# Kernel optimization log

Measured on AMD Instinct MI355X. Metric: run time of the kernel, lower is better.

The kernel has to match this reference:

```python
import jax, jax.numpy as jnp
import numpy as np

# hyperparameters (from init_kwargs / repo defaults)
AMP_COEF = 1.0
ARG_COEF = 1.0
SSIM_COEF = 1.0
BETA = 1.0
STFT_COEF = 1e-4
EPS = 1e-8
STFT_F = 12
STFT_S = 4


def _gauss_kernel(size=11, sigma=1.5):
    x = jnp.arange(size, dtype=jnp.float32) - (size - 1) / 2.0
    g = jnp.exp(-0.5 * (x / sigma) ** 2)
    k = jnp.outer(g, g)
    return k / jnp.sum(k)


def _depthwise_filter(img, k):
    # img: [B,H,W,C]; 11x11 gaussian, VALID padding, depthwise (per-channel)
    c = img.shape[-1]
    kern = jnp.tile(k[:, :, None, None], (1, 1, 1, c))  # HWIO, I=1, O=C
    return jax.lax.conv_general_dilated(
        img, kern, (1, 1), 'VALID',
        dimension_numbers=('NHWC', 'HWIO', 'NHWC'),
        feature_group_count=c)


def ssim(x, y, max_val=1.0):
    # faithful to tf.image.ssim defaults: filter 11, sigma 1.5, k1=0.01, k2=0.03
    c1 = (0.01 * max_val) ** 2
    c2 = (0.03 * max_val) ** 2
    k = _gauss_kernel()
    mu_x = _depthwise_filter(x, k)
    mu_y = _depthwise_filter(y, k)
    var_x = _depthwise_filter(x * x, k) - mu_x * mu_x
    var_y = _depthwise_filter(y * y, k) - mu_y * mu_y
    cov = _depthwise_filter(x * y, k) - mu_x * mu_y
    lum = (2.0 * mu_x * mu_y + c1) / (mu_x * mu_x + mu_y * mu_y + c1)
    cs = (2.0 * cov + c2) / (var_x + var_y + c2)
    return jnp.mean(lum * cs, axis=(1, 2, 3))  # [B]


def stft(image, f=STFT_F, s=STFT_S):
    # image: [B,N,N,C] -> batched patchwise 2D FFT, cropped to [:f//2,:f//2]
    n = image.shape[1]
    p = (n - f) // s + 1          # num_conv per axis
    half = f // 2
    rows = (jnp.arange(p) * s)[:, None] + jnp.arange(f)   # [P, f]
    patches = image[:, rows]                              # [B,P,f,N,C]
    patches = patches[:, :, :, rows]                      # [B,P,f,P,f,C]
    patches = jnp.transpose(patches, (0, 1, 3, 2, 4, 5))  # [B,Pi,Pj,f,f,C]
    b, c = image.shape[0], image.shape[-1]
    patches = patches.reshape(b, p * p, f, f, c)          # k = i*P + j ordering
    fft = jnp.fft.fft2(patches.astype(jnp.complex64), axes=(2, 3))
    return fft[:, :, :half, :half, :]                     # [B,P*P,half,half,C]


def _freq_filter(f=STFT_F):
    lin = jnp.linspace(0.0, 1.0, f // 2)[:, None]
    return (lin * lin.T)[:, :, None]                      # [half,half,1]


def setup_inputs() -> dict:
    key = jax.random.key(0)
    k1, k2, k3, k4 = jax.random.split(key, 4)
    B, N, C, L = 32, 160, 3, 128
    return {
        'mean': jax.random.normal(k1, (B, L), dtype=jnp.float32),
        'logvar': jax.random.normal(k2, (B, L), dtype=jnp.float32),
        'x_in': jax.random.uniform(k3, (B, N, N, C), dtype=jnp.float32),
        'x_out': jax.random.uniform(k4, (B, N, N, C), dtype=jnp.float32),
    }


def reference(mean, logvar, x_in, x_out):
    # KLD per sample
    var = jnp.exp(logvar)
    kld = -0.5 * jnp.sum(1.0 + logvar - var - mean * mean, axis=1)  # [B]
    # SSIM recon term
    recons = SSIM_COEF * ssim(x_in, x_out, 1.0)                     # [B]
    # patchwise STFT amp/phase loss ('ours')
    stft_out = stft(x_out, STFT_F, STFT_S)
    stft_in = stft(x_in, STFT_F, STFT_S)
    ff = _freq_filter(STFT_F)                                       # [half,half,1]
    arg_diff = jnp.abs(jnp.angle(stft_out + EPS) - jnp.angle(stft_in + EPS))
    amp_diff = jnp.abs(jnp.abs(stft_out) - jnp.abs(stft_in))
    arg_loss = jnp.sum(arg_diff * ff, axis=(1, 2, 3, 4))            # [B]
    amp_loss = jnp.sum(amp_diff * ff, axis=(1, 2, 3, 4))            # [B]
    stft_loss = ARG_COEF * arg_loss + AMP_COEF * amp_loss
    loss = jnp.mean(BETA * kld + recons + STFT_COEF * stft_loss)
    return loss
```

## Files before the change

kernel.cpp:

```cpp
#include <hip/hip_runtime.h>
#include <hip/hip_fp16.h>
#include <math.h>

#define BATCH 32
#define NPIX 160
#define LDIM 128
#define OUT_SZ 150

#define THREADS 512
#define N_BLOCKS 1825
#define SCRATCH_OFF 2880
#define VSTRIDE 1296
#define SMEM_FLOATS 9360

__device__ constexpr float TWC[12] = { 1.f, 0.86602540f, 0.5f, 0.f, -0.5f, -0.86602540f,
                                      -1.f,-0.86602540f,-0.5f, 0.f,  0.5f,  0.86602540f};
__device__ constexpr float TWS[12] = { 0.f,-0.5f,-0.86602540f,-1.f,-0.86602540f,-0.5f,
                                       0.f, 0.5f, 0.86602540f, 1.f, 0.86602540f, 0.5f};

__device__ constexpr float GW[11] = {0.00102838f, 0.00759876f, 0.03600076f, 0.10936070f,
                                     0.21300554f, 0.26601172f, 0.21300554f, 0.10936070f,
                                     0.03600076f, 0.00759876f, 0.00102838f};

__device__ __forceinline__ float fast_atan2f(float y, float x) {
    float ax = fabsf(x), ay = fabsf(y);
    float mx = fmaxf(ax, ay), mn = fminf(ax, ay);
    float z = mn * __builtin_amdgcn_rcpf(mx);
    float z2 = z * z;
    float p = fmaf(z2, -0.01172120f, 0.05265332f);
    p = fmaf(z2, p, -0.11643287f);
    p = fmaf(z2, p, 0.19354346f);
    p = fmaf(z2, p, -0.33262347f);
    p = fmaf(z2, p, 0.99997726f);
    p = p * z;
    if (ay > ax) p = 1.57079632679489662f - p;
    if (x < 0.f) p = 3.14159265358979323f - p;
    return (y < 0.f) ? -p : p;
}

__device__ __forceinline__ float4 extract_c(float4 f0, float4 f1, float4 f2, int c) {
    if (c == 0) return make_float4(f0.x, f0.w, f1.z, f2.y);
    if (c == 1) return make_float4(f0.y, f1.x, f1.w, f2.z);
    return make_float4(f0.z, f1.y, f2.x, f2.w);
}

__global__ __launch_bounds__(THREADS) void work_kernel(const float* __restrict__ xin,
                                                       const float* __restrict__ xout,
                                                       const float* __restrict__ mean,
                                                       const float* __restrict__ logvar,
                                                       float* __restrict__ out) {
    __shared__ __align__(16) float SMEM[SMEM_FLOATS];
    __shared__ float sm8[8];
    const int tid = threadIdx.x;
    const int gid = blockIdx.x;
    float acc = 0.f;

    if (gid == 1824) {
        float a = 0.f;
        for (int i = tid; i < BATCH * LDIM; i += THREADS) {
            float m = mean[i], lv = logvar[i];
            a += -0.5f * (1.f + lv - expf(lv) - m * m) * (1.f / 32.f);
        }
        #pragma unroll
        for (int o = 32; o > 0; o >>= 1) a += __shfl_down(a, o, 64);
        if ((tid & 63) == 0) sm8[tid >> 6] = a;
        __syncthreads();
        if (tid == 0) {
            float s = sm8[0];
            #pragma unroll
            for (int i = 1; i < 8; ++i) s += sm8[i];
            atomicAdd(out, s);
        }
        return;
    }

    int b    = gid / 57;
    int rem  = gid % 57;
    int c    = rem / 19;
    int tile = rem % 19;
    int r0 = tile * 8;
    __half2* HXY = (__half2*)SMEM;
    __half2* RD  = (__half2*)(SMEM + SCRATCH_OFF);

    for (int t = tid; t < 720; t += THREADS) {
        int rr = t / 40;
        int cq = t % 40;
        int row = r0 + rr;
        float4 xa = make_float4(0.f, 0.f, 0.f, 0.f);
        float4 xb = make_float4(0.f, 0.f, 0.f, 0.f);
        if (row < NPIX) {
            size_t off = ((size_t)(b * 160 + row) * 160 + cq * 4) * 3;
            const float4* qa = (const float4*)(xin + off);
            const float4* qb = (const float4*)(xout + off);
            float4 a0 = qa[0], a1 = qa[1], a2 = qa[2];
            float4 b0 = qb[0], b1 = qb[1], b2 = qb[2];
            xa = extract_c(a0, a1, a2, c);
            xb = extract_c(b0, b1, b2, c);
        }
        __half2 h[4] __attribute__((aligned(16)));
        h[0] = __floats2half2_rn(xa.x, xb.x);
        h[1] = __floats2half2_rn(xa.y, xb.y);
        h[2] = __floats2half2_rn(xa.z, xb.z);
        h[3] = __floats2half2_rn(xa.w, xb.w);
        *(float4*)&HXY[rr * 160 + cq * 4] = *(float4*)h;
    }
    __syncthreads();

    for (int t = tid; t < 608; t += THREADS) {
        int pc = t % 38;
        int r  = t / 38;
        float4 raw[3];
        raw[0] = *(const float4*)&HXY[r * 160 + pc * 4];
        raw[1] = *(const float4*)&HXY[r * 160 + pc * 4 + 4];
        raw[2] = *(const float4*)&HXY[r * 160 + pc * 4 + 8];
        const __half2* hp = (const __half2*)raw;
        float xa[12], xb[12];
        #pragma unroll
        for (int j = 0; j < 12; ++j) {
            float2 xy = __half22float2(hp[j]);
            xa[j] = xy.x; xb[j] = xy.y;
        }
        float evA[5] = {xa[1]+xa[11], xa[2]+xa[10], xa[3]+xa[9], xa[4]+xa[8], xa[5]+xa[7]};
        float ovA[5] = {xa[1]-xa[11], xa[2]-xa[10], xa[3]-xa[9], xa[4]-xa[8], xa[5]-xa[7]};
        float evB[5] = {xb[1]+xb[11], xb[2]+xb[10], xb[3]+xb[9], xb[4]+xb[8], xb[5]+xb[7]};
        float ovB[5] = {xb[1]-xb[11], xb[2]-xb[10], xb[3]-xb[9], xb[4]-xb[8], xb[5]-xb[7]};
        #pragma unroll
        for (int vv = 0; vv < 5; ++vv) {
            int v = vv + 1;
            float reA = xa[0] + ((v & 1) ? -xa[6] : xa[6]);
            float reB = xb[0] + ((v & 1) ? -xb[6] : xb[6]);
            float imA = 0.f, imB = 0.f;
            #pragma unroll
            for (int j = 1; j <= 5; ++j) {
                int kk = (v * j) % 12;
                reA = fmaf(evA[j-1], TWC[kk], reA);
                imA = fmaf(ovA[j-1], TWS[kk], imA);
                reB = fmaf(evB[j-1], TWC[kk], reB);
                imB = fmaf(ovB[j-1], TWS[kk], imB);
            }
            __half2 w2[2] __attribute__((aligned(8)));
            w2[0] = __floats2half2_rn(reA, imA);
            w2[1] = __floats2half2_rn(reB, imB);
            *(float2*)&RD[(((r * 5 + vv) * 38) + pc) * 2] = *(float2*)w2;
        }
    }
    __syncthreads();

    if (tid < 380) {
        int pc = tid % 38;
        int vv = (tid / 38) % 5;
        int g  = tid / 190;
        float FR0[5] = {0,0,0,0,0}, FI0[5] = {0,0,0,0,0};
        float FR1[5] = {0,0,0,0,0}, FI1[5] = {0,0,0,0,0};
        #pragma unroll
        for (int i = 0; i < 6; ++i) {
            int rlo = 4 * g + i, rhi = rlo + 6;
            __half2 p0[2] __attribute__((aligned(8)));
            __half2 p6[2] __attribute__((aligned(8)));
            *(float2*)p0 = *(const float2*)&RD[(((rlo * 5 + vv) * 38) + pc) * 2];
            *(float2*)p6 = *(const float2*)&RD[(((rhi * 5 + vv) * 38) + pc) * 2];
            float2 a0 = __half22float2(p0[0]);
            float2 b0 = __half22float2(p0[1]);
            float2 a6 = __half22float2(p6[0]);
            float2 b6 = __half22float2(p6[1]);
            float spR0 = a0.x + a6.x, spI0 = a0.y + a6.y;
            float smR0 = a0.x - a6.x, smI0 = a0.y - a6.y;
            float spR1 = b0.x + b6.x, spI1 = b0.y + b6.y;
            float smR1 = b0.x - b6.x, smI1 = b0.y - b6.y;
            #pragma unroll
            for (int uu = 0; uu < 5; ++uu) {
                int u = uu + 1;
                int kk = (u * i) % 12;
                float cu = TWC[kk], su = TWS[kk];
                float sR0 = (u & 1) ? smR0 : spR0, sI0 = (u & 1) ? smI0 : spI0;
                float sR1 = (u & 1) ? smR1 : spR1, sI1 = (u & 1) ? smI1 : spI1;
                FR0[uu] = fmaf(cu, sR0, fmaf(-su, sI0, FR0[uu]));
                FI0[uu] = fmaf(cu, sI0, fmaf( su, sR0, FI0[uu]));
                FR1[uu] = fmaf(cu, sR1, fmaf(-su, sI1, FR1[uu]));
                FI1[uu] = fmaf(cu, sI1, fmaf( su, sR1, FI1[uu]));
            }
        }
        float sacc = 0.f;
        #pragma unroll
        for (int uu = 0; uu < 5; ++uu) {
            float aI = fast_atan2f(FI0[uu], FR0[uu] + 1e-8f);
            float aO = fast_atan2f(FI1[uu], FR1[uu] + 1e-8f);
            float mI = __builtin_amdgcn_sqrtf(fmaf(FR0[uu], FR0[uu], FI0[uu] * FI0[uu]));
            float mO = __builtin_amdgcn_sqrtf(fmaf(FR1[uu], FR1[uu], FI1[uu] * FI1[uu]));
            float ff = (float)((uu + 1) * (vv + 1)) * 0.04f;
            sacc += ff * (fabsf(aO - aI) + fabsf(mO - mI));
        }
        acc += sacc * (1e-4f / 32.f);
    }
    __syncthreads();

    for (int t = tid; t < 320; t += THREADS) {
        int orow = t / 40;
        int cbase = (t % 40) * 4;
        float ax[4] = {0,0,0,0}, ay[4] = {0,0,0,0};
        float axx[4] = {0,0,0,0}, ayy[4] = {0,0,0,0}, axy[4] = {0,0,0,0};
        #pragma unroll
        for (int kk = 0; kk < 11; ++kk) {
            float4 raw = *(const float4*)&HXY[(orow + kk) * 160 + cbase];
            const __half2* hp = (const __half2*)&raw;
            float wg = GW[kk];
            #pragma unroll
            for (int o = 0; o < 4; ++o) {
                float2 xy = __half22float2(hp[o]);
                float tx = wg * xy.x, ty = wg * xy.y;
                ax[o]  += tx;
                ay[o]  += ty;
                axx[o] = fmaf(tx, xy.x, axx[o]);
                ayy[o] = fmaf(ty, xy.y, ayy[o]);
                axy[o] = fmaf(tx, xy.y, axy[o]);
            }
        }
        int base = SCRATCH_OFF + orow * 160 + cbase;
        *(float4*)&SMEM[base + 0 * VSTRIDE] = make_float4(ax[0],  ax[1],  ax[2],  ax[3]);
        *(float4*)&SMEM[base + 1 * VSTRIDE] = make_float4(ay[0],  ay[1],  ay[2],  ay[3]);
        *(float4*)&SMEM[base + 2 * VSTRIDE] = make_float4(axx[0], axx[1], axx[2], axx[3]);
        *(float4*)&SMEM[base + 3 * VSTRIDE] = make_float4(ayy[0], ayy[1], ayy[2], ayy[3]);
        *(float4*)&SMEM[base + 4 * VSTRIDE] = make_float4(axy[0], axy[1], axy[2], axy[3]);
    }
    __syncthreads();

    {
        float hacc = 0.f;
        for (int t = tid; t < 600; t += THREADS) {
            int orow = t / 75;
            int oc = (t % 75) * 2;
            float st[5][2];
            #pragma unroll
            for (int p = 0; p < 5; ++p) {
                const float* rowp = &SMEM[SCRATCH_OFF + p * VSTRIDE + orow * 160 + oc];
                float vals[12];
                #pragma unroll
                for (int q = 0; q < 6; ++q) {
                    float2 v2 = *(const float2*)&rowp[2 * q];
                    vals[2 * q]     = v2.x;
                    vals[2 * q + 1] = v2.y;
                }
                float s0 = 0.f, s1 = 0.f;
                #pragma unroll
                for (int kk = 0; kk < 11; ++kk) {
                    s0 += GW[kk] * vals[kk];
                    s1 += GW[kk] * vals[kk + 1];
                }
                st[p][0] = s0; st[p][1] = s1;
            }
            const float c1 = 1e-4f, c2 = 9e-4f;
            if (r0 + orow < OUT_SZ) {
                #pragma unroll
                for (int o = 0; o < 2; ++o) {
                    float mx = st[0][o], my = st[1][o];
                    float vx = st[2][o] - mx * mx;
                    float vy = st[3][o] - my * my;
                    float cv = st[4][o] - mx * my;
                    float lum = (2.f * mx * my + c1) *
                                __builtin_amdgcn_rcpf(fmaf(mx, mx, my * my) + c1);
                    float cs  = (2.f * cv + c2) *
                                __builtin_amdgcn_rcpf(vx + vy + c2);
                    hacc += lum * cs;
                }
            }
        }
        acc += hacc * (1.f / (32.f * 150.f * 150.f * 3.f));
    }

    #pragma unroll
    for (int o = 32; o > 0; o >>= 1) acc += __shfl_down(acc, o, 64);
    if ((tid & 63) == 0) sm8[tid >> 6] = acc;
    __syncthreads();
    if (tid == 0) {
        float s = sm8[0];
        #pragma unroll
        for (int i = 1; i < 8; ++i) s += sm8[i];
        atomicAdd(out, s);
    }
}

extern "C" void kernel_launch(void* const* d_in, const int* in_sizes, int n_in,
                              void* d_out, int out_size, void* d_ws, size_t ws_size,
                              hipStream_t stream) {
    const float* mean   = (const float*)d_in[0];
    const float* logvar = (const float*)d_in[1];
    const float* xin    = (const float*)d_in[2];
    const float* xout   = (const float*)d_in[3];
    float* out = (float*)d_out;

    hipMemsetAsync(out, 0, sizeof(float), stream);
    work_kernel<<<N_BLOCKS, THREADS, 0, stream>>>(xin, xout, mean, logvar, out);
}
```

Before: 116.9 us.

## Overlap SSIM vertical pass with STFT row DFT and pack intermediates in half

Moves the SSIM vertical Gaussian pass into the same barrier phase as the STFT row DFT, using reversed thread indices so otherwise idle high threads do it. This removes one __syncthreads and lets the STFT column pass and the SSIM horizontal pass share a phase. The vertical-pass mean and second-moment sums are now stored as packed half2 in a separate shared region with a padded row stride, while the covariance sum stays fp32. This costs more shared memory (12896 floats) and lowers precision on the variance terms, which can hurt SSIM accuracy through cancellation.

```diff
diff --git a/kernel.cpp b/kernel.cpp
--- a/kernel.cpp
+++ b/kernel.cpp
@@ -9,9 +9,12 @@
 
 #define THREADS 512
 #define N_BLOCKS 1825
-#define SCRATCH_OFF 2880
-#define VSTRIDE 1296
-#define SMEM_FLOATS 9360
+#define RD_OFF   2880
+#define VPMU_OFF 8960
+#define VPVV_OFF 10272
+#define VPXY_OFF 11584
+#define VROWSTR  164
+#define SMEM_FLOATS 12896
 
 __device__ constexpr float TWC[12] = { 1.f, 0.86602540f, 0.5f, 0.f, -0.5f, -0.86602540f,
                                       -1.f,-0.86602540f,-0.5f, 0.f,  0.5f,  0.86602540f};
@@ -80,7 +83,7 @@
     int tile = rem % 19;
     int r0 = tile * 8;
     __half2* HXY = (__half2*)SMEM;
-    __half2* RD  = (__half2*)(SMEM + SCRATCH_OFF);
+    __half2* RD  = (__half2*)(SMEM + RD_OFF);
 
     for (int t = tid; t < 720; t += THREADS) {
         int rr = t / 40;
@@ -106,6 +109,7 @@
     }
     __syncthreads();
 
+
     for (int t = tid; t < 608; t += THREADS) {
         int pc = t % 38;
         int r  = t / 38;
@@ -144,7 +148,45 @@
             *(float2*)&RD[(((r * 5 + vv) * 38) + pc) * 2] = *(float2*)w2;
         }
     }
+
+    {
+        int vt = (THREADS - 1) - tid;
+        if (vt < 320) {
+            int orow = vt / 40;
+            int cbase = (vt % 40) * 4;
+            float ax[4] = {0,0,0,0}, ay[4] = {0,0,0,0};
+            float axx[4] = {0,0,0,0}, ayy[4] = {0,0,0,0}, axy[4] = {0,0,0,0};
+            #pragma unroll
+            for (int kk = 0; kk < 11; ++kk) {
+                float4 raw = *(const float4*)&HXY[(orow + kk) * 160 + cbase];
+                const __half2* hp = (const __half2*)&raw;
+                float wg = GW[kk];
+                #pragma unroll
+                for (int o = 0; o < 4; ++o) {
+                    float2 xy = __half22float2(hp[o]);
+                    float tx = wg * xy.x, ty = wg * xy.y;
+                    ax[o]  += tx;
+                    ay[o]  += ty;
+                    axx[o] = fmaf(tx, xy.x, axx[o]);
+                    ayy[o] = fmaf(ty, xy.y, ayy[o]);
+                    axy[o] = fmaf(tx, xy.y, axy[o]);
+                }
+            }
+            __half2 pm[4] __attribute__((aligned(16)));
+            __half2 pv[4] __attribute__((aligned(16)));
+            #pragma unroll
+            for (int o = 0; o < 4; ++o) {
+                pm[o] = __floats2half2_rn(ax[o],  ay[o]);
+                pv[o] = __floats2half2_rn(axx[o], ayy[o]);
+            }
+            int base = orow * VROWSTR + cbase;
+            *(float4*)&SMEM[VPMU_OFF + base] = *(float4*)pm;
+            *(float4*)&SMEM[VPVV_OFF + base] = *(float4*)pv;
+            *(float4*)&SMEM[VPXY_OFF + base] = make_float4(axy[0], axy[1], axy[2], axy[3]);
+        }
+    }
     __syncthreads();
+
 
     if (tid < 380) {
         int pc = tid % 38;
@@ -192,70 +234,78 @@
         }
         acc += sacc * (1e-4f / 32.f);
     }
-    __syncthreads();
-
-    for (int t = tid; t < 320; t += THREADS) {
-        int orow = t / 40;
-        int cbase = (t % 40) * 4;
-        float ax[4] = {0,0,0,0}, ay[4] = {0,0,0,0};
-        float axx[4] = {0,0,0,0}, ayy[4] = {0,0,0,0}, axy[4] = {0,0,0,0};
-        #pragma unroll
-        for (int kk = 0; kk < 11; ++kk) {
-            float4 raw = *(const float4*)&HXY[(orow + kk) * 160 + cbase];
-            const __half2* hp = (const __half2*)&raw;
-            float wg = GW[kk];
-            #pragma unroll
-            for (int o = 0; o < 4; ++o) {
-                float2 xy = __half22float2(hp[o]);
-                float tx = wg * xy.x, ty = wg * xy.y;
-                ax[o]  += tx;
-                ay[o]  += ty;
-                axx[o] = fmaf(tx, xy.x, axx[o]);
-                ayy[o] = fmaf(ty, xy.y, ayy[o]);
-                axy[o] = fmaf(tx, xy.y, axy[o]);
-            }
-        }
-        int base = SCRATCH_OFF + orow * 160 + cbase;
-        *(float4*)&SMEM[base + 0 * VSTRIDE] = make_float4(ax[0],  ax[1],  ax[2],  ax[3]);
-        *(float4*)&SMEM[base + 1 * VSTRIDE] = make_float4(ay[0],  ay[1],  ay[2],  ay[3]);
-        *(float4*)&SMEM[base + 2 * VSTRIDE] = make_float4(axx[0], axx[1], axx[2], axx[3]);
-        *(float4*)&SMEM[base + 3 * VSTRIDE] = make_float4(ayy[0], ayy[1], ayy[2], ayy[3]);
-        *(float4*)&SMEM[base + 4 * VSTRIDE] = make_float4(axy[0], axy[1], axy[2], axy[3]);
-    }
-    __syncthreads();
 
     {
         float hacc = 0.f;
-        for (int t = tid; t < 600; t += THREADS) {
+        for (int t = (THREADS - 1) - tid; t < 600; t += THREADS) {
             int orow = t / 75;
             int oc = (t % 75) * 2;
-            float st[5][2];
-            #pragma unroll
-            for (int p = 0; p < 5; ++p) {
-                const float* rowp = &SMEM[SCRATCH_OFF + p * VSTRIDE + orow * 160 + oc];
-                float vals[12];
+            int base = orow * VROWSTR + oc;
+            float mx0, mx1, my0, my1, xx0, xx1, yy0, yy1, xy0, xy1;
+            {
+                float xs[12], ys[12];
                 #pragma unroll
                 for (int q = 0; q < 6; ++q) {
-                    float2 v2 = *(const float2*)&rowp[2 * q];
-                    vals[2 * q]     = v2.x;
-                    vals[2 * q + 1] = v2.y;
-                }
-                float s0 = 0.f, s1 = 0.f;
+                    float2 m2 = *(const float2*)&SMEM[VPMU_OFF + base + 2 * q];
+                    const __half2* mh = (const __half2*)&m2;
+                    float2 a = __half22float2(mh[0]), bb = __half22float2(mh[1]);
+                    xs[2*q] = a.x;  ys[2*q] = a.y;
+                    xs[2*q+1] = bb.x; ys[2*q+1] = bb.y;
+                }
+                float s0=0.f, s1=0.f, s2=0.f, s3=0.f;
                 #pragma unroll
                 for (int kk = 0; kk < 11; ++kk) {
-                    s0 += GW[kk] * vals[kk];
-                    s1 += GW[kk] * vals[kk + 1];
-                }
-                st[p][0] = s0; st[p][1] = s1;
-            }
-            const float c1 = 1e-4f, c2 = 9e-4f;
+                    s0 = fmaf(GW[kk], xs[kk],   s0);
+                    s1 = fmaf(GW[kk], xs[kk+1], s1);
+                    s2 = fmaf(GW[kk], ys[kk],   s2);
+                    s3 = fmaf(GW[kk], ys[kk+1], s3);
+                }
+                mx0 = s0; mx1 = s1; my0 = s2; my1 = s3;
+            }
+            {
+                float xs[12], ys[12];
+                #pragma unroll
+                for (int q = 0; q < 6; ++q) {
+                    float2 v2 = *(const float2*)&SMEM[VPVV_OFF + base + 2 * q];
+                    const __half2* vh = (const __half2*)&v2;
+                    float2 a = __half22float2(vh[0]), bb = __half22float2(vh[1]);
+                    xs[2*q] = a.x;  ys[2*q] = a.y;
+                    xs[2*q+1] = bb.x; ys[2*q+1] = bb.y;
+                }
+                float s0=0.f, s1=0.f, s2=0.f, s3=0.f;
+                #pragma unroll
+                for (int kk = 0; kk < 11; ++kk) {
+                    s0 = fmaf(GW[kk], xs[kk],   s0);
+                    s1 = fmaf(GW[kk], xs[kk+1], s1);
+                    s2 = fmaf(GW[kk], ys[kk],   s2);
+                    s3 = fmaf(GW[kk], ys[kk+1], s3);
+                }
+                xx0 = s0; xx1 = s1; yy0 = s2; yy1 = s3;
+            }
+            {
+                float zs[12];
+                #pragma unroll
+                for (int q = 0; q < 6; ++q) {
+                    float2 y2 = *(const float2*)&SMEM[VPXY_OFF + base + 2 * q];
+                    zs[2*q] = y2.x; zs[2*q+1] = y2.y;
+                }
+                float s0=0.f, s1=0.f;
+                #pragma unroll
+                for (int kk = 0; kk < 11; ++kk) {
+                    s0 = fmaf(GW[kk], zs[kk],   s0);
+                    s1 = fmaf(GW[kk], zs[kk+1], s1);
+                }
+                xy0 = s0; xy1 = s1;
+            }
             if (r0 + orow < OUT_SZ) {
+                const float c1 = 1e-4f, c2 = 9e-4f;
                 #pragma unroll
                 for (int o = 0; o < 2; ++o) {
-                    float mx = st[0][o], my = st[1][o];
-                    float vx = st[2][o] - mx * mx;
-                    float vy = st[3][o] - my * my;
-                    float cv = st[4][o] - mx * my;
+                    float mx = o ? mx1 : mx0, my = o ? my1 : my0;
+                    float ex = o ? xx1 : xx0, ey = o ? yy1 : yy0;
+                    float cv = (o ? xy1 : xy0) - mx * my;
+                    float vx = ex - mx * mx;
+                    float vy = ey - my * my;
                     float lum = (2.f * mx * my + c1) *
                                 __builtin_amdgcn_rcpf(fmaf(mx, mx, my * my) + c1);
                     float cs  = (2.f * cv + c2) *
```

Result: faster. 114.0 us (-2.4%).
